# Kernel tuning notes

Measured on AMD Instinct MI355X. Metric: run time of the kernel, lower is better.

## Reference

```python
import jax, jax.numpy as jnp
import numpy as np

B = 2048          # number of graphs in the batch
ACT_DIM = 14      # nodes per graph (act_dim)
C = 128           # in_channels
H = 256           # hidden_size


def _pair_edges(n):
    ii, jj = np.meshgrid(np.arange(n), np.arange(n), indexing='ij')
    m = ii != jj
    return np.stack([ii[m], jj[m]], axis=1)  # [n*(n-1), 2]


def setup_inputs() -> dict:
    key = jax.random.key(0)
    ks = jax.random.split(key, 12)
    edges_np = _pair_edges(ACT_DIM)                       # [182, 2]
    offs = (np.arange(B) * ACT_DIM)[:, None, None]
    batched = (edges_np[None] + offs).reshape(-1, 2)      # [B*182, 2]
    edge_index = jnp.asarray(batched.T, dtype=jnp.int64 if jax.config.jax_enable_x64 else jnp.int32)
    edges = jnp.asarray(edges_np, dtype=jnp.int32)

    def lin(k, o, i):
        return jax.random.normal(k, (o, i), jnp.float32) * (1.0 / np.sqrt(i))

    return {
        'state': jax.random.normal(ks[0], (B * ACT_DIM, C), jnp.float32),
        'conv_w': lin(ks[1], C, C),
        'conv_b': jnp.zeros((C,), jnp.float32),
        'lin1_w': lin(ks[2], H, 2 * C),
        'lin1_b': jax.random.normal(ks[3], (H,), jnp.float32) * 0.01,
        'lin2_w': lin(ks[4], H, H),
        'lin2_b': jax.random.normal(ks[5], (H,), jnp.float32) * 0.01,
        'mu_w': lin(ks[6], 1, H),
        'mu_b': jnp.zeros((1,), jnp.float32),
        'sig_w': lin(ks[7], 1, H),
        'sig_b': jnp.zeros((1,), jnp.float32),
        'noise': jax.random.normal(ks[8], (B, edges_np.shape[0]), jnp.float32),
        'edge_index': edge_index,
        'edges': edges,
    }


def _gcn_conv(x, edge_index, w, b):
    # Standard GCNConv: add self-loops, symmetric normalization, x @ W^T, scatter-add, + bias.
    n = x.shape[0]
    loops = jnp.arange(n, dtype=edge_index.dtype)
    src = jnp.concatenate([edge_index[0], loops])
    dst = jnp.concatenate([edge_index[1], loops])
    deg = jax.ops.segment_sum(jnp.ones_like(src, dtype=x.dtype), dst, num_segments=n)
    dinv = jax.lax.rsqrt(deg)  # deg >= 1 because of self-loops
    norm = dinv[src] * dinv[dst]                       # [E+N]
    xw = x @ w.T                                       # [N, C]
    msg = xw[src] * norm[:, None]                      # gather + scale
    return jax.ops.segment_sum(msg, dst, num_segments=n) + b


def reference(state, conv_w, conv_b, lin1_w, lin1_b, lin2_w, lin2_b,
              mu_w, mu_b, sig_w, sig_b, noise, edge_index, edges):
    out = jax.nn.relu(_gcn_conv(state, edge_index, conv_w, conv_b))
    x = (out + state).reshape(-1, ACT_DIM, C)          # [B, 14, C]
    es, ed = edges[:, 0], edges[:, 1]
    ef = jnp.concatenate([x[:, es, :], x[:, ed, :]], axis=2)   # [B, E, 2C]
    h = jax.nn.leaky_relu(jnp.einsum('bec,hc->beh', ef, lin1_w) + lin1_b)
    h = jax.nn.leaky_relu(jnp.einsum('beh,gh->beg', h, lin2_w) + lin2_b)
    mu = jax.nn.softplus(jnp.einsum('beh,oh->beo', h, mu_w) + mu_b)[..., 0]   # [B, E]
    std = jax.nn.softplus(jnp.einsum('beh,oh->beo', h, sig_w) + sig_b)[..., 0]
    action = mu + std * noise                          # Normal rsample with fixed eps
    log_prob = jnp.sum(
        -0.5 * ((action - mu) / std) ** 2 - jnp.log(std) - 0.5 * jnp.log(2.0 * jnp.pi),
        axis=-1)                                       # [B]
    return action, log_prob
```

## Files before the change

### kernel.cpp

```cpp
#include <hip/hip_runtime.h>
#include <hip/hip_bf16.h>

#define ACT 14
#define CC 128
#define HH 256
#define EPB 182
#define NB 2048
#define M2 (NB*EPB)
#define NS 520
#define LP_CONST (-182.0f * 0.91893853320467274f)

typedef short s16x8 __attribute__((ext_vector_type(8)));
typedef float f32x4 __attribute__((ext_vector_type(4)));
typedef float f32x16 __attribute__((ext_vector_type(16)));

__device__ __forceinline__ short f2bf(float f) {
    unsigned u = __float_as_uint(f);
    unsigned r = (u + 0x7fffu + ((u >> 16) & 1u)) >> 16;
    return (short)r;
}
__device__ __forceinline__ float b2f(short s) {
    return __uint_as_float(((unsigned)(unsigned short)s) << 16);
}
__device__ __forceinline__ float bflo(int m) { return __uint_as_float(((unsigned)m) << 16); }
__device__ __forceinline__ float bfhi(int m) { return __uint_as_float((unsigned)m & 0xffff0000u); }
__device__ __forceinline__ float leaky(float x) { return fmaxf(x, 0.01f * x); }
__device__ __forceinline__ float softplusf(float x) { return x > 15.f ? x : log1pf(expf(x)); }

union bf2u { __hip_bfloat162 h; int i; };
__device__ __forceinline__ int pk_bf16(float a, float b) {
    bf2u u; u.h = __float22bfloat162_rn(make_float2(a, b));
    return u.i;
}

__global__ __launch_bounds__(256) void prep_kernel(
    const float* __restrict__ conv_w, const float* __restrict__ lin1_w,
    const float* __restrict__ lin2_w,
    short* __restrict__ W2bf, short* __restrict__ W1bf,
    short* __restrict__ cwTbf, short* __restrict__ w1sTbf)
{
    int i = blockIdx.x * 256 + threadIdx.x;
    W2bf[i] = f2bf(lin2_w[i]);
    {
        int n = i >> 7, k = i & 127;
        float v = (n < 256) ? lin1_w[n * 256 + k] : lin1_w[(n - 256) * 256 + 128 + k];
        W1bf[i] = f2bf(v);
    }
    if (i < 16384) {
        int k = i >> 7, j = i & 127;
        cwTbf[i] = f2bf(conv_w[j * 128 + k]);
    }
    if (i < 32768) {
        int k = i >> 8, h = i & 255;
        w1sTbf[i] = f2bf(lin1_w[h * 256 + k] + lin1_w[h * 256 + 128 + k]);
    }
}

__global__ __launch_bounds__(512, 4) void actor_kernel(
    const float* __restrict__ state, const short* __restrict__ W1bf,
    const short* __restrict__ W2bf,
    const short* __restrict__ cwTbf, const float* __restrict__ conv_b,
    const short* __restrict__ w1sTbf, const float* __restrict__ lin1_b,
    const float* __restrict__ lin2_b, const float* __restrict__ mu_w,
    const float* __restrict__ mu_b, const float* __restrict__ sig_w,
    const float* __restrict__ sig_b, const float* __restrict__ noise,
    const int* __restrict__ edges, float* __restrict__ out)
{
    __shared__ short stateL[4 * 16 * 40];
    __shared__ short h1L[2][16 * 512];
    __shared__ short nodeL[ACT * NS];
    __shared__ float ssumL[128], gL[128], wL[256];
    __shared__ float b2L[256], muL[256], sgL[256];
    __shared__ float mu_acc[192], sg_acc[192];
    __shared__ float lp_acc;

    const int t = threadIdx.x, b = blockIdx.x;
    const int lane = t & 63, ln = lane & 15, q = lane >> 4;
    const int w = t >> 6;
    const int l32 = lane & 31, hf = lane >> 5;

    {
        int row = t >> 5, c4 = t & 31;
        int kk = c4 >> 3, k8 = (c4 & 7) * 4;
        int* dst = (int*)&stateL[kk * 640 + row * 40 + k8];
        if (row < ACT) {
            f32x4 x = *(const f32x4*)(state + ((size_t)b * ACT + row) * CC + c4 * 4);
            dst[0] = pk_bf16(x[0], x[1]); dst[1] = pk_bf16(x[2], x[3]);
        } else { dst[0] = 0; dst[1] = 0; }
    }
    if (t < 256) { b2L[t] = lin2_b[t]; muL[t] = mu_w[t]; sgL[t] = sig_w[t]; }
    if (t >= 256 && t < 384) {
        int c = t - 256;
        const float* sp = state + (size_t)b * ACT * CC + c;
        float s = 0.f;
        #pragma unroll
        for (int r = 0; r < ACT; ++r) s += sp[r * CC];
        ssumL[c] = s * (1.f / 14.f);
    }
    if (t < 192) { mu_acc[t] = 0.f; sg_acc[t] = 0.f; }
    if (t == 0) lp_acc = 0.f;
    __syncthreads();

    if (t < 128) {
        float a = 0.f;
        #pragma unroll 8
        for (int k = 0; k < 128; ++k) a += b2f(cwTbf[k * 128 + t]) * ssumL[k];
        gL[t] = fmaxf(a + conv_b[t], 0.f);
    }
    __syncthreads();
    if (t < 256) {
        float a = 0.f;
        #pragma unroll 8
        for (int k = 0; k < 128; ++k) a += b2f(w1sTbf[k * 256 + t]) * gL[k];
        wL[t] = a + lin1_b[t];
    }
    __syncthreads();

    f32x4 zero4 = {0.f, 0.f, 0.f, 0.f};
    f32x4 nacc[4];
    nacc[0] = zero4; nacc[1] = zero4; nacc[2] = zero4; nacc[3] = zero4;
    #pragma unroll
    for (int c = 0; c < 4; ++c) {
        s16x8 a8 = *(const s16x8*)&stateL[c * 640 + ln * 40 + q * 8];
        #pragma unroll
        for (int i = 0; i < 4; ++i) {
            int ct = w + 8 * i;
            s16x8 b8 = *(const s16x8*)&W1bf[(size_t)(ct * 16 + ln) * CC + c * 32 + q * 8];
            nacc[i] = __builtin_amdgcn_mfma_f32_16x16x32_bf16(a8, b8, nacc[i], 0, 0, 0);
        }
    }
    #pragma unroll
    for (int i = 0; i < 4; ++i) {
        int col = (w + 8 * i) * 16 + ln;
        float wadd = (col < HH) ? wL[col] : 0.f;
        #pragma unroll
        for (int rg = 0; rg < 4; ++rg) {
            int node = q * 4 + rg;
            if (node < ACT) nodeL[node * NS + col] = f2bf(nacc[i][rg] + wadd);
        }
    }

    s16x8 wa[16];
    #pragma unroll
    for (int c = 0; c < 16; ++c)
        wa[c] = *(const s16x8*)&W2bf[(size_t)(w * 32 + l32) * HH + c * 16 + hf * 8];
    __syncthreads();

    auto build = [&](int tile, int bufi) {
        int e32 = t & 31;
        int e = tile * 32 + e32;
        bool ok = e < EPB;
        int uo = 0, vo = 0;
        if (ok) { int2 p = ((const int2*)edges)[e]; uo = p.x * NS; vo = p.y * NS + HH; }
        int sl = t >> 5;
        #pragma unroll
        for (int s = 0; s < 2; ++s) {
            int slot = sl + 16 * s;
            int chunk = slot >> 1, half = slot & 1;
            int koff = chunk * 16 + half * 8;
            int o[4] = {0, 0, 0, 0};
            if (ok) {
                s16x8 u8 = *(const s16x8*)&nodeL[uo + koff];
                s16x8 v8 = *(const s16x8*)&nodeL[vo + koff];
                const int* ui = (const int*)&u8;
                const int* vi = (const int*)&v8;
                #pragma unroll
                for (int j = 0; j < 4; ++j) {
                    int uu = ui[j], vv = vi[j];
                    float s0 = bflo(uu) + bflo(vv);
                    float s1 = bfhi(uu) + bfhi(vv);
                    o[j] = pk_bf16(leaky(s0), leaky(s1));
                }
            }
            *(s16x8*)&h1L[bufi][chunk * 512 + (half * 32 + e32) * 8] = *(const s16x8*)o;
        }
    };

    build(0, 0);
    for (int tile = 0; tile < 6; ++tile) {
        __syncthreads();
        if (tile < 5) build(tile + 1, (tile + 1) & 1);
        const int buf = tile & 1;
        f32x16 acc;
        #pragma unroll
        for (int r = 0; r < 16; ++r) acc[r] = 0.f;
        #pragma unroll
        for (int c = 0; c < 16; ++c) {
            s16x8 b8 = *(const s16x8*)&h1L[buf][c * 512 + lane * 8];
            acc = __builtin_amdgcn_mfma_f32_32x32x16_bf16(wa[c], b8, acc, 0, 0, 0);
        }
        float pmu = 0.f, psg = 0.f;
        const int ns = w * 32;
        #pragma unroll
        for (int r = 0; r < 16; ++r) {
            int n = ns + (r & 3) + 8 * (r >> 2) + 4 * hf;
            float h2 = leaky(acc[r] + b2L[n]);
            pmu += muL[n] * h2;
            psg += sgL[n] * h2;
        }
        pmu += __shfl_xor(pmu, 32);
        psg += __shfl_xor(psg, 32);
        if (l32 == lane) {
            atomicAdd(&mu_acc[tile * 32 + l32], pmu);
            atomicAdd(&sg_acc[tile * 32 + l32], psg);
        }
    }
    __syncthreads();

    float lpv = 0.f;
    if (t < EPB) {
        float mu = softplusf(mu_acc[t] + mu_b[0]);
        float sd = softplusf(sg_acc[t] + sig_b[0]);
        float z = noise[(size_t)b * EPB + t];
        out[(size_t)b * EPB + t] = mu + sd * z;
        lpv = -0.5f * z * z - logf(sd);
    }
    if (w < 3) {
        #pragma unroll
        for (int off = 1; off < 64; off <<= 1) lpv += __shfl_xor(lpv, off);
        if (lane == 0) atomicAdd(&lp_acc, lpv);
    }
    __syncthreads();
    if (t == 0) out[M2 + b] = lp_acc + LP_CONST;
}

extern "C" void kernel_launch(void* const* d_in, const int* in_sizes, int n_in,
                              void* d_out, int out_size, void* d_ws, size_t ws_size,
                              hipStream_t stream)
{
    const float* state  = (const float*)d_in[0];
    const float* conv_w = (const float*)d_in[1];
    const float* conv_b = (const float*)d_in[2];
    const float* lin1_w = (const float*)d_in[3];
    const float* lin1_b = (const float*)d_in[4];
    const float* lin2_w = (const float*)d_in[5];
    const float* lin2_b = (const float*)d_in[6];
    const float* mu_w   = (const float*)d_in[7];
    const float* mu_b   = (const float*)d_in[8];
    const float* sig_w  = (const float*)d_in[9];
    const float* sig_b  = (const float*)d_in[10];
    const float* noise  = (const float*)d_in[11];
    const int*   edges  = (const int*)d_in[13];
    float* out = (float*)d_out;

    char* ws = (char*)d_ws;
    short* W2bf   = (short*)ws;  ws += 65536 * 2;
    short* W1bf   = (short*)ws;  ws += 65536 * 2;
    short* cwTbf  = (short*)ws;  ws += 16384 * 2;
    short* w1sTbf = (short*)ws;  ws += 32768 * 2;

    prep_kernel<<<256, 256, 0, stream>>>(conv_w, lin1_w, lin2_w,
                                         W2bf, W1bf, cwTbf, w1sTbf);
    actor_kernel<<<NB, 512, 0, stream>>>(state, W1bf, W2bf,
                                         cwTbf, conv_b, w1sTbf, lin1_b,
                                         lin2_b, mu_w, mu_b, sig_w, sig_b,
                                         noise, edges, out);
}
```

Measured before the change: 237.2 us.

## Process two graphs per block to amortize per-block setup and weight loads

```diff
diff --git a/kernel.cpp b/kernel.cpp
--- a/kernel.cpp
+++ b/kernel.cpp
@@ -66,79 +66,107 @@
     const float* __restrict__ sig_b, const float* __restrict__ noise,
     const int* __restrict__ edges, float* __restrict__ out)
 {
-    __shared__ short stateL[4 * 16 * 40];
-    __shared__ short h1L[2][16 * 512];
-    __shared__ short nodeL[ACT * NS];
-    __shared__ float ssumL[128], gL[128], wL[256];
+    __shared__ short h1L[2][8192];
+    __shared__ short nodeL[2 * ACT * NS];
+    __shared__ float ssumL[2][128];
+    __shared__ float gL[2][128];
+    __shared__ float wL[2][256];
     __shared__ float b2L[256], muL[256], sgL[256];
-    __shared__ float mu_acc[192], sg_acc[192];
-    __shared__ float lp_acc;
+    __shared__ float mu_acc[384], sg_acc[384];
+    __shared__ float lp_acc[2];
+
+    short* stateL = &h1L[0][0];
+    float* pp     = (float*)&h1L[0][5120];
 
     const int t = threadIdx.x, b = blockIdx.x;
     const int lane = t & 63, ln = lane & 15, q = lane >> 4;
     const int w = t >> 6;
     const int l32 = lane & 31, hf = lane >> 5;
 
-    {
-        int row = t >> 5, c4 = t & 31;
+    #pragma unroll
+    for (int it = 0; it < 2; ++it) {
+        int idx = it * 512 + t;
+        int bt = idx >> 9, row = (idx >> 5) & 15, c4 = idx & 31;
         int kk = c4 >> 3, k8 = (c4 & 7) * 4;
-        int* dst = (int*)&stateL[kk * 640 + row * 40 + k8];
+        int* dst = (int*)&stateL[bt * 2560 + kk * 640 + row * 40 + k8];
         if (row < ACT) {
-            f32x4 x = *(const f32x4*)(state + ((size_t)b * ACT + row) * CC + c4 * 4);
+            f32x4 x = *(const f32x4*)(state + ((size_t)(2 * b + bt) * ACT + row) * CC + c4 * 4);
             dst[0] = pk_bf16(x[0], x[1]); dst[1] = pk_bf16(x[2], x[3]);
         } else { dst[0] = 0; dst[1] = 0; }
     }
     if (t < 256) { b2L[t] = lin2_b[t]; muL[t] = mu_w[t]; sgL[t] = sig_w[t]; }
-    if (t >= 256 && t < 384) {
-        int c = t - 256;
-        const float* sp = state + (size_t)b * ACT * CC + c;
+    else {
+        int i = t - 256, bt = i >> 7, c = i & 127;
+        const float* sp = state + (size_t)(2 * b + bt) * ACT * CC + c;
         float s = 0.f;
         #pragma unroll
         for (int r = 0; r < ACT; ++r) s += sp[r * CC];
-        ssumL[c] = s * (1.f / 14.f);
-    }
-    if (t < 192) { mu_acc[t] = 0.f; sg_acc[t] = 0.f; }
-    if (t == 0) lp_acc = 0.f;
-    __syncthreads();
-
-    if (t < 128) {
+        ssumL[bt][c] = s * (1.f / 14.f);
+    }
+    if (t < 384) { mu_acc[t] = 0.f; sg_acc[t] = 0.f; }
+    if (t < 2) lp_acc[t] = 0.f;
+    __syncthreads();
+
+    {
+        int bt = t >> 8, s = (t >> 7) & 1, j = t & 127;
+        const float* ss = ssumL[bt];
         float a = 0.f;
         #pragma unroll 8
-        for (int k = 0; k < 128; ++k) a += b2f(cwTbf[k * 128 + t]) * ssumL[k];
-        gL[t] = fmaxf(a + conv_b[t], 0.f);
+        for (int kk = 0; kk < 64; ++kk) {
+            int k = s * 64 + kk;
+            a += b2f(cwTbf[k * 128 + j]) * ss[k];
+        }
+        pp[t] = a;
     }
     __syncthreads();
     if (t < 256) {
+        int bt = t >> 7, j = t & 127;
+        float a = pp[bt * 256 + j] + pp[bt * 256 + 128 + j] + conv_b[j];
+        gL[bt][j] = fmaxf(a, 0.f);
+    }
+    __syncthreads();
+    {
+        int bt = t >> 8, h = t & 255;
+        const float* gg = gL[bt];
         float a = 0.f;
         #pragma unroll 8
-        for (int k = 0; k < 128; ++k) a += b2f(w1sTbf[k * 256 + t]) * gL[k];
-        wL[t] = a + lin1_b[t];
+        for (int k = 0; k < 128; ++k)
+            a += b2f(w1sTbf[k * 256 + h]) * gg[k];
+        wL[bt][h] = a + lin1_b[h];
     }
     __syncthreads();
 
     f32x4 zero4 = {0.f, 0.f, 0.f, 0.f};
-    f32x4 nacc[4];
-    nacc[0] = zero4; nacc[1] = zero4; nacc[2] = zero4; nacc[3] = zero4;
+    f32x4 nacc[2][4];
+    #pragma unroll
+    for (int bt = 0; bt < 2; ++bt) {
+        nacc[bt][0] = zero4; nacc[bt][1] = zero4;
+        nacc[bt][2] = zero4; nacc[bt][3] = zero4;
+    }
     #pragma unroll
     for (int c = 0; c < 4; ++c) {
-        s16x8 a8 = *(const s16x8*)&stateL[c * 640 + ln * 40 + q * 8];
+        s16x8 a80 = *(const s16x8*)&stateL[0 * 2560 + c * 640 + ln * 40 + q * 8];
+        s16x8 a81 = *(const s16x8*)&stateL[1 * 2560 + c * 640 + ln * 40 + q * 8];
         #pragma unroll
         for (int i = 0; i < 4; ++i) {
             int ct = w + 8 * i;
             s16x8 b8 = *(const s16x8*)&W1bf[(size_t)(ct * 16 + ln) * CC + c * 32 + q * 8];
-            nacc[i] = __builtin_amdgcn_mfma_f32_16x16x32_bf16(a8, b8, nacc[i], 0, 0, 0);
-        }
-    }
-    #pragma unroll
-    for (int i = 0; i < 4; ++i) {
-        int col = (w + 8 * i) * 16 + ln;
-        float wadd = (col < HH) ? wL[col] : 0.f;
-        #pragma unroll
-        for (int rg = 0; rg < 4; ++rg) {
-            int node = q * 4 + rg;
-            if (node < ACT) nodeL[node * NS + col] = f2bf(nacc[i][rg] + wadd);
-        }
-    }
+            nacc[0][i] = __builtin_amdgcn_mfma_f32_16x16x32_bf16(a80, b8, nacc[0][i], 0, 0, 0);
+            nacc[1][i] = __builtin_amdgcn_mfma_f32_16x16x32_bf16(a81, b8, nacc[1][i], 0, 0, 0);
+        }
+    }
+    #pragma unroll
+    for (int bt = 0; bt < 2; ++bt)
+        #pragma unroll
+        for (int i = 0; i < 4; ++i) {
+            int col = (w + 8 * i) * 16 + ln;
+            float wadd = (col < HH) ? wL[bt][col] : 0.f;
+            #pragma unroll
+            for (int rg = 0; rg < 4; ++rg) {
+                int node = q * 4 + rg;
+                if (node < ACT) nodeL[(bt * ACT + node) * NS + col] = f2bf(nacc[bt][i][rg] + wadd);
+            }
+        }
 
     s16x8 wa[16];
     #pragma unroll
@@ -147,11 +175,13 @@
     __syncthreads();
 
     auto build = [&](int tile, int bufi) {
+        int bt = (tile >= 6) ? 1 : 0;
         int e32 = t & 31;
-        int e = tile * 32 + e32;
+        int e = (tile - bt * 6) * 32 + e32;
         bool ok = e < EPB;
-        int uo = 0, vo = 0;
-        if (ok) { int2 p = ((const int2*)edges)[e]; uo = p.x * NS; vo = p.y * NS + HH; }
+        int base = bt * ACT * NS;
+        int uo = base, vo = base + HH;
+        if (ok) { int2 p = ((const int2*)edges)[e]; uo += p.x * NS; vo += p.y * NS; }
         int sl = t >> 5;
         #pragma unroll
         for (int s = 0; s < 2; ++s) {
@@ -177,9 +207,9 @@
     };
 
     build(0, 0);
-    for (int tile = 0; tile < 6; ++tile) {
+    for (int tile = 0; tile < 12; ++tile) {
         __syncthreads();
-        if (tile < 5) build(tile + 1, (tile + 1) & 1);
+        if (tile < 11) build(tile + 1, (tile + 1) & 1);
         const int buf = tile & 1;
         f32x16 acc;
         #pragma unroll
@@ -189,39 +219,42 @@
             s16x8 b8 = *(const s16x8*)&h1L[buf][c * 512 + lane * 8];
             acc = __builtin_amdgcn_mfma_f32_32x32x16_bf16(wa[c], b8, acc, 0, 0, 0);
         }
+        int bt = (tile >= 6) ? 1 : 0;
+        int col0 = (tile - bt * 6) * 32;
         float pmu = 0.f, psg = 0.f;
-        const int ns = w * 32;
+        const int nsb = w * 32;
         #pragma unroll
         for (int r = 0; r < 16; ++r) {
-            int n = ns + (r & 3) + 8 * (r >> 2) + 4 * hf;
+            int n = nsb + (r & 3) + 8 * (r >> 2) + 4 * hf;
             float h2 = leaky(acc[r] + b2L[n]);
             pmu += muL[n] * h2;
             psg += sgL[n] * h2;
         }
         pmu += __shfl_xor(pmu, 32);
         psg += __shfl_xor(psg, 32);
-        if (l32 == lane) {
-            atomicAdd(&mu_acc[tile * 32 + l32], pmu);
-            atomicAdd(&sg_acc[tile * 32 + l32], psg);
+        if (lane < 32) {
+            atomicAdd(&mu_acc[bt * 192 + col0 + l32], pmu);
+            atomicAdd(&sg_acc[bt * 192 + col0 + l32], psg);
         }
     }
     __syncthreads();
 
     float lpv = 0.f;
-    if (t < EPB) {
-        float mu = softplusf(mu_acc[t] + mu_b[0]);
-        float sd = softplusf(sg_acc[t] + sig_b[0]);
-        float z = noise[(size_t)b * EPB + t];
-        out[(size_t)b * EPB + t] = mu + sd * z;
-        lpv = -0.5f * z * z - logf(sd);
-    }
-    if (w < 3) {
-        #pragma unroll
-        for (int off = 1; off < 64; off <<= 1) lpv += __shfl_xor(lpv, off);
-        if (lane == 0) atomicAdd(&lp_acc, lpv);
-    }
-    __syncthreads();
-    if (t == 0) out[M2 + b] = lp_acc + LP_CONST;
+    {
+        int bt = t >> 8, i = t & 255;
+        if (i < EPB) {
+            float mu = softplusf(mu_acc[bt * 192 + i] + mu_b[0]);
+            float sd = softplusf(sg_acc[bt * 192 + i] + sig_b[0]);
+            float z = noise[(size_t)(2 * b + bt) * EPB + i];
+            out[(size_t)(2 * b + bt) * EPB + i] = mu + sd * z;
+            lpv = -0.5f * z * z - logf(sd);
+        }
+    }
+    #pragma unroll
+    for (int off = 1; off < 64; off <<= 1) lpv += __shfl_xor(lpv, off);
+    if (lane == 0) atomicAdd(&lp_acc[t >> 8], lpv);
+    __syncthreads();
+    if (t < 2) out[M2 + 2 * b + t] = lp_acc[t] + LP_CONST;
 }
 
 extern "C" void kernel_launch(void* const* d_in, const int* in_sizes, int n_in,
@@ -251,8 +284,8 @@
 
     prep_kernel<<<256, 256, 0, stream>>>(conv_w, lin1_w, lin2_w,
                                          W2bf, W1bf, cwTbf, w1sTbf);
-    actor_kernel<<<NB, 512, 0, stream>>>(state, W1bf, W2bf,
-                                         cwTbf, conv_b, w1sTbf, lin1_b,
-                                         lin2_b, mu_w, mu_b, sig_w, sig_b,
-                                         noise, edges, out);
-}
+    actor_kernel<<<NB / 2, 512, 0, stream>>>(state, W1bf, W2bf,
+                                             cwTbf, conv_b, w1sTbf, lin1_b,
+                                             lin2_b, mu_w, mu_b, sig_w, sig_b,
+                                             noise, edges, out);
+}
```

After: 211.6 us. 10.8% less time.
